# Optimization experiments

Measured on AMD Instinct MI355X. Metric: run time of the kernel, lower is better.

## Reference

```python
import jax, jax.numpy as jnp
import numpy as np

B, N, M = 8, 512, 6          # batch, num_roads, max_action
ED, SRC, OBS = 8, 64, 32     # edge_dim, source_obs_dim, obs_dim
D, H = 16, 64                # out_dim (fixed in source), MLPBase hidden


def setup_inputs() -> dict:
    key = jax.random.key(0)
    ks = jax.random.split(key, 24)
    p = lambda k, sh, s=0.05: (jax.random.normal(k, sh) * s).astype(jnp.float32)
    inp = {}
    inp['obs'] = jax.random.normal(ks[0], (B, SRC), dtype=jnp.float32)
    inp['obs_all'] = jax.random.normal(ks[1], (B, N, OBS), dtype=jnp.float32)
    inp['edge_attrs'] = jax.random.normal(ks[2], (B, N, N, ED), dtype=jnp.float32)
    inp['ridxs'] = jax.random.randint(ks[3], (B,), 0, N)
    idxs = jax.random.randint(ks[4], (N, M), 0, N)
    masks = jax.random.randint(ks[5], (N, M), 0, 2)
    inp['road_neighbor_idxs'] = idxs
    inp['road_neighbor_masks'] = masks
    # A[i, j] = 1 iff i is a (masked-valid) neighbor of j
    cols = jnp.repeat(jnp.arange(N), M)
    inp['A'] = jnp.zeros((N, N), jnp.float32).at[idxs.reshape(-1), cols].max(
        masks.reshape(-1).astype(jnp.float32))
    inp['PA'] = jnp.full((N, N), 1e-6, jnp.float32)
    # parameters (stored as (in, out); y = x @ W + b)
    inp['w_src'] = p(ks[6], (SRC, D * M)); inp['b_src'] = jnp.zeros((D * M,), jnp.float32)
    inp['w_obs'] = p(ks[7], (OBS, D));     inp['b_obs'] = jnp.zeros((D,), jnp.float32)
    inp['res_w'] = p(ks[8], (2, D, D));    inp['res_b'] = jnp.zeros((2, D), jnp.float32)
    inp['ge_we'] = p(ks[9], (2, ED, D));   inp['ge_be'] = jnp.zeros((2, D), jnp.float32)
    inp['ge_wemb'] = p(ks[10], (2, 3 * D, D)); inp['ge_bemb'] = jnp.zeros((2, D), jnp.float32)
    inp['gated_w'] = p(ks[11], (2 * D * M, 2 * D)); inp['gated_b'] = jnp.zeros((2 * D,), jnp.float32)
    inp['base_w1'] = p(ks[12], (D, H));    inp['base_b1'] = jnp.zeros((H,), jnp.float32)
    inp['base_w2'] = p(ks[13], (H, H));    inp['base_b2'] = jnp.zeros((H,), jnp.float32)
    inp['act_w'] = p(ks[14], (H, M));      inp['act_b'] = jnp.zeros((M,), jnp.float32)
    return inp


def _edge_conv_gat(x, edge_attrs, adj, we, be, wemb, bemb):
    """EdgeConvGat: emb(cat[x_i, x_j, edge_map(e)]) aggregated by adj.
    emb is linear, so split its weight and avoid the (B,N,N,3D) concat:
      sum_j adj[bij] * (x_i W1 + x_j W2 + e_ij W3 + b)
    """
    W1, W2, W3 = wemb[:D], wemb[D:2 * D], wemb[2 * D:]
    e = edge_attrs @ we + be                      # (B,N,N,D)
    ep = e @ W3                                   # (B,N,N,D)
    deg = adj.sum(-1)                             # (B,N) row-sums of adj
    return ((x @ W1) * deg[..., None]
            + jnp.einsum('bij,bjk->bik', adj, x @ W2)
            + jnp.einsum('bij,bijk->bik', adj, ep)
            + bemb * deg[..., None])


def reference(obs, obs_all, edge_attrs, ridxs, road_neighbor_idxs,
              road_neighbor_masks, A, PA, w_src, b_src, w_obs, b_obs,
              res_w, res_b, ge_we, ge_be, ge_wemb, ge_bemb,
              gated_w, gated_b, base_w1, base_b1, base_w2, base_b2,
              act_w, act_b):
    # source_obs_map / obs_map (mean_field=1 -> full obs_all)
    obs_p = obs @ w_src + b_src                   # (B, D*M)
    x = obs_all @ w_obs + b_obs                   # (B, N, D)
    # adaptive adjacency (training=False -> dropout is identity)
    adj = jnp.broadcast_to(A + PA, (obs.shape[0], N, N))
    # graph conv loop (source overwrites obs_all_adaptive each iter from the
    # same x, faithfully reproduced; only the last iteration feeds the output)
    x_adapt = x
    for i in range(2):
        res = x @ res_w[i] + res_b[i]
        agg = _edge_conv_gat(x, edge_attrs, adj, ge_we[i], ge_be[i],
                             ge_wemb[i], ge_bemb[i])
        x_adapt = jax.nn.relu(res + agg)
    # gather per-road neighbor features and mask invalid slots to -1
    idx = road_neighbor_idxs[ridxs]               # (B, M)
    mask = road_neighbor_masks[ridxs]             # (B, M)
    sel = jnp.take_along_axis(x_adapt, idx[:, :, None], axis=1)  # (B, M, D)
    sel = jnp.where(mask[..., None] == 0, -1.0, sel).reshape(obs.shape[0], -1)
    # gated fusion + MLPBase (2-layer MLP stand-in) + action head
    g = jnp.concatenate([obs_p, sel], axis=-1) @ gated_w + gated_b
    gated, gate = jnp.split(g, 2, axis=-1)
    h = gated * jax.nn.sigmoid(gate)
    h = jax.nn.relu(h @ base_w1 + base_b1)
    h = jax.nn.relu(h @ base_w2 + base_b2)        # F.relu(self.base(...))
    return h @ act_w + act_b                      # (B, M) action values
```

## Files before the change

kernel.cpp:

```cpp
#include <hip/hip_runtime.h>
#include <math.h>


constexpr int Bc   = 8;
constexpr int Nc   = 512;
constexpr int Mc   = 6;
constexpr int EDc  = 8;
constexpr int SRCc = 64;
constexpr int OBSc = 32;
constexpr int Dc   = 16;
constexpr int Hc   = 64;

__global__ __launch_bounds__(512) void anmodel_kernel(
    const float* __restrict__ obs,
    const float* __restrict__ obs_all,
    const float* __restrict__ edge_attrs,
    const int*   __restrict__ ridxs,
    const int*   __restrict__ rni,
    const int*   __restrict__ rnm,
    const float* __restrict__ A,
    const float* __restrict__ PA,
    const float* __restrict__ w_src,
    const float* __restrict__ b_src,
    const float* __restrict__ w_obs,
    const float* __restrict__ b_obs,
    const float* __restrict__ res_w,
    const float* __restrict__ res_b,
    const float* __restrict__ ge_we,
    const float* __restrict__ ge_be,
    const float* __restrict__ ge_wemb,
    const float* __restrict__ ge_bemb,
    const float* __restrict__ gated_w,
    const float* __restrict__ gated_b,
    const float* __restrict__ base_w1,
    const float* __restrict__ base_b1,
    const float* __restrict__ base_w2,
    const float* __restrict__ base_b2,
    const float* __restrict__ act_w,
    const float* __restrict__ act_b,
    float* __restrict__ out)
{
    const int b    = blockIdx.x;
    const int tid  = threadIdx.x;
    const int lane = tid & 63;
    const int wave = tid >> 6;

    __shared__ float s_y[Nc][Dc];
    __shared__ float s_wobs[OBSc][Dc];
    __shared__ float s_bobs[Dc];
    __shared__ float s_W1[Dc][Dc];
    __shared__ float s_W2[Dc][Dc];
    __shared__ float s_resw[Dc][Dc];
    __shared__ float s_resb[Dc];
    __shared__ float s_we3[EDc][Dc];
    __shared__ float s_be3[Dc];
    __shared__ float s_bemb[Dc];
    __shared__ float s_sel[Mc * Dc];
    __shared__ float s_obsp[SRCc + 32];
    __shared__ float s_h0[Dc];
    __shared__ float s_h1[Hc];
    __shared__ float s_h2[Hc];

    const float* wemb1 = ge_wemb + 3 * Dc * Dc;
    for (int t = tid; t < OBSc * Dc; t += 512) s_wobs[t / Dc][t % Dc] = w_obs[t];
    for (int t = tid; t < Dc; t += 512) {
        s_bobs[t] = b_obs[t];
        s_resb[t] = res_b[Dc + t];
        s_bemb[t] = ge_bemb[Dc + t];
        float acc = 0.f;
        #pragma unroll
        for (int k = 0; k < Dc; ++k)
            acc = fmaf(ge_be[Dc + k], wemb1[(2 * Dc + k) * Dc + t], acc);
        s_be3[t] = acc;
    }
    for (int t = tid; t < Dc * Dc; t += 512) {
        s_W1[t / Dc][t % Dc]   = wemb1[t];
        s_W2[t / Dc][t % Dc]   = wemb1[Dc * Dc + t];
        s_resw[t / Dc][t % Dc] = res_w[Dc * Dc + t];
    }
    for (int t = tid; t < EDc * Dc; t += 512) {
        const int e = t / Dc, d = t % Dc;
        float acc = 0.f;
        #pragma unroll
        for (int k = 0; k < Dc; ++k)
            acc = fmaf(ge_we[EDc * Dc + e * Dc + k], wemb1[(2 * Dc + k) * Dc + d], acc);
        s_we3[e][d] = acc;
    }
    __syncthreads();

    {
        const int j = tid;
        const float* oa = obs_all + ((size_t)b * Nc + j) * OBSc;
        float o[OBSc];
        #pragma unroll
        for (int k = 0; k < OBSc; k += 4) {
            const float4 v = *reinterpret_cast<const float4*>(oa + k);
            o[k] = v.x; o[k + 1] = v.y; o[k + 2] = v.z; o[k + 3] = v.w;
        }
        float xv[Dc];
        #pragma unroll
        for (int d = 0; d < Dc; ++d) xv[d] = s_bobs[d];
        #pragma unroll
        for (int k = 0; k < OBSc; ++k) {
            const float ok = o[k];
            #pragma unroll
            for (int d = 0; d < Dc; ++d) xv[d] = fmaf(ok, s_wobs[k][d], xv[d]);
        }
        #pragma unroll
        for (int d = 0; d < Dc; ++d) {
            float acc = 0.f;
            #pragma unroll
            for (int k = 0; k < Dc; ++k) acc = fmaf(xv[k], s_W2[k][d], acc);
            s_y[j][d] = acc;
        }
    }
    __syncthreads();

    if (wave < Mc) {
        const int m  = wave;
        const int r  = ridxs[b];
        const int i  = rni[r * Mc + m];
        const int mk = rnm[r * Mc + m];
        const float* Arow = A  + (size_t)i * Nc;
        const float* Prow = PA + (size_t)i * Nc;

        float dv = 0.f;
        #pragma unroll
        for (int t = 0; t < 8; ++t) {
            const int j = lane * 8 + t;
            dv += Arow[j] + Prow[j];
        }
        #pragma unroll
        for (int s = 1; s < 64; s <<= 1) dv += __shfl_xor(dv, s);

        const int dq = lane & 15, jg = lane >> 4;
        float adot = 0.f;
        for (int t = 0; t < Nc / 4; ++t) {
            const int j = t * 4 + jg;
            adot = fmaf(Arow[j] + Prow[j], s_y[j][dq], adot);
        }
        adot += __shfl_xor(adot, 16);
        adot += __shfl_xor(adot, 32);

        const int e8 = lane & 7, jg8 = lane >> 3;
        const float* Erow = edge_attrs + (((size_t)b * Nc + i) * Nc) * EDc;
        float ag = 0.f;
        for (int t = 0; t < Nc / 8; ++t) {
            const int j = t * 8 + jg8;
            ag = fmaf(Arow[j] + Prow[j], Erow[(size_t)j * EDc + e8], ag);
        }
        ag += __shfl_xor(ag, 8);
        ag += __shfl_xor(ag, 16);
        ag += __shfl_xor(ag, 32);
        float agv[EDc];
        #pragma unroll
        for (int e = 0; e < EDc; ++e) agv[e] = __shfl(ag, e);

        const float* oa = obs_all + ((size_t)b * Nc + i) * OBSc;
        float xi[Dc];
        #pragma unroll
        for (int d = 0; d < Dc; ++d) xi[d] = s_bobs[d];
        for (int k = 0; k < OBSc; ++k) {
            const float ok = oa[k];
            #pragma unroll
            for (int d = 0; d < Dc; ++d) xi[d] = fmaf(ok, s_wobs[k][d], xi[d]);
        }

        if (lane < Dc) {
            const int d = lane;
            float resv = s_resb[d];
            float w1t  = 0.f;
            #pragma unroll
            for (int k = 0; k < Dc; ++k) {
                resv = fmaf(xi[k], s_resw[k][d], resv);
                w1t  = fmaf(xi[k], s_W1[k][d], w1t);
            }
            float agdot = 0.f;
            #pragma unroll
            for (int e = 0; e < EDc; ++e) agdot = fmaf(agv[e], s_we3[e][d], agdot);
            float aggv = fmaf(w1t, dv, adot) + agdot + dv * s_be3[d] + s_bemb[d] * dv;
            float xa = resv + aggv;
            xa = xa > 0.f ? xa : 0.f;
            s_sel[m * Dc + d] = (mk == 0) ? -1.0f : xa;
        }
    } else if (wave == 6) {
        for (int t = lane; t < SRCc + 32; t += 64) {
            float acc = b_src[t];
            for (int s = 0; s < SRCc; ++s)
                acc = fmaf(obs[b * SRCc + s], w_src[s * 96 + t], acc);
            s_obsp[t] = acc;
        }
    }
    __syncthreads();

    if (wave == 0) {
        float gv = 0.f;
        if (lane < 32) {
            gv = gated_b[lane];
            for (int t = 0; t < 96; ++t) gv = fmaf(s_obsp[t], gated_w[t * 32 + lane], gv);
            for (int t = 0; t < 96; ++t) gv = fmaf(s_sel[t],  gated_w[(96 + t) * 32 + lane], gv);
        }
        const float gate = __shfl(gv, (lane & 15) + 16);
        if (lane < Dc) {
            s_h0[lane] = gv * (1.0f / (1.0f + expf(-gate)));
        }
    }
    __syncthreads();
    if (wave == 0) {
        float acc = base_b1[lane];
        #pragma unroll
        for (int k = 0; k < Dc; ++k) acc = fmaf(s_h0[k], base_w1[k * Hc + lane], acc);
        s_h1[lane] = acc > 0.f ? acc : 0.f;
    }
    __syncthreads();
    if (wave == 0) {
        float acc = base_b2[lane];
        #pragma unroll
        for (int k = 0; k < Hc; ++k) acc = fmaf(s_h1[k], base_w2[k * Hc + lane], acc);
        s_h2[lane] = acc > 0.f ? acc : 0.f;
    }
    __syncthreads();
    if (wave == 0 && lane < Mc) {
        float acc = act_b[lane];
        #pragma unroll
        for (int k = 0; k < Hc; ++k) acc = fmaf(s_h2[k], act_w[k * Mc + lane], acc);
        out[b * Mc + lane] = acc;
    }
}

extern "C" void kernel_launch(void* const* d_in, const int* in_sizes, int n_in,
                              void* d_out, int out_size, void* d_ws, size_t ws_size,
                              hipStream_t stream) {
    (void)in_sizes; (void)n_in; (void)d_ws; (void)ws_size; (void)out_size;
    anmodel_kernel<<<dim3(Bc), dim3(512), 0, stream>>>(
        (const float*)d_in[0],  (const float*)d_in[1],  (const float*)d_in[2],
        (const int*)  d_in[3],  (const int*)  d_in[4],  (const int*)  d_in[5],
        (const float*)d_in[6],  (const float*)d_in[7],  (const float*)d_in[8],
        (const float*)d_in[9],  (const float*)d_in[10], (const float*)d_in[11],
        (const float*)d_in[12], (const float*)d_in[13], (const float*)d_in[14],
        (const float*)d_in[15], (const float*)d_in[16], (const float*)d_in[17],
        (const float*)d_in[18], (const float*)d_in[19], (const float*)d_in[20],
        (const float*)d_in[21], (const float*)d_in[22], (const float*)d_in[23],
        (const float*)d_in[24], (const float*)d_in[25],
        (float*)d_out);
}
```

Measured before the change: 160.1 us.

## Stage adjacency rows in LDS and defer W2 projection after aggregation

All threads now load the six needed A+PA rows into shared memory with coalesced reads, replacing the repeated per-wave global reads of A and PA. Node features x are stored directly, and the W2 projection is applied once to the aggregated vector instead of per node, so each thread skips a 16x16 matvec. The x_i recompute reuses s_x instead of reloading obs_all. The obs projection is spread over two waves, and several loops get unroll pragmas. This adds a 12KB shared buffer and a few extra shuffles.

```diff
diff --git a/kernel.cpp b/kernel.cpp
--- a/kernel.cpp
+++ b/kernel.cpp
@@ -45,7 +45,8 @@
     const int lane = tid & 63;
     const int wave = tid >> 6;
 
-    __shared__ float s_y[Nc][Dc];
+    __shared__ float s_x[Nc][Dc];
+    __shared__ float s_w[Mc][Nc];
     __shared__ float s_wobs[OBSc][Dc];
     __shared__ float s_bobs[Dc];
     __shared__ float s_W1[Dc][Dc];
@@ -55,6 +56,8 @@
     __shared__ float s_we3[EDc][Dc];
     __shared__ float s_be3[Dc];
     __shared__ float s_bemb[Dc];
+    __shared__ int   s_idx[Mc];
+    __shared__ int   s_msk[Mc];
     __shared__ float s_sel[Mc * Dc];
     __shared__ float s_obsp[SRCc + 32];
     __shared__ float s_h0[Dc];
@@ -86,6 +89,11 @@
             acc = fmaf(ge_we[EDc * Dc + e * Dc + k], wemb1[(2 * Dc + k) * Dc + d], acc);
         s_we3[e][d] = acc;
     }
+    if (tid < Mc) {
+        const int r = ridxs[b];
+        s_idx[tid] = rni[r * Mc + tid];
+        s_msk[tid] = rnm[r * Mc + tid];
+    }
     __syncthreads();
 
     {
@@ -107,47 +115,46 @@
             for (int d = 0; d < Dc; ++d) xv[d] = fmaf(ok, s_wobs[k][d], xv[d]);
         }
         #pragma unroll
-        for (int d = 0; d < Dc; ++d) {
-            float acc = 0.f;
-            #pragma unroll
-            for (int k = 0; k < Dc; ++k) acc = fmaf(xv[k], s_W2[k][d], acc);
-            s_y[j][d] = acc;
-        }
+        for (int d = 0; d < Dc; ++d) s_x[j][d] = xv[d];
+    }
+    #pragma unroll
+    for (int m = 0; m < Mc; ++m) {
+        const int i = s_idx[m];
+        s_w[m][tid] = A[(size_t)i * Nc + tid] + PA[(size_t)i * Nc + tid];
     }
     __syncthreads();
 
     if (wave < Mc) {
-        const int m  = wave;
-        const int r  = ridxs[b];
-        const int i  = rni[r * Mc + m];
-        const int mk = rnm[r * Mc + m];
-        const float* Arow = A  + (size_t)i * Nc;
-        const float* Prow = PA + (size_t)i * Nc;
+        const int m = wave;
+        const float* __restrict__ wrow = &s_w[m][0];
 
         float dv = 0.f;
         #pragma unroll
-        for (int t = 0; t < 8; ++t) {
-            const int j = lane * 8 + t;
-            dv += Arow[j] + Prow[j];
-        }
+        for (int t = 0; t < Nc / 64; ++t) dv += wrow[t * 64 + lane];
         #pragma unroll
         for (int s = 1; s < 64; s <<= 1) dv += __shfl_xor(dv, s);
 
         const int dq = lane & 15, jg = lane >> 4;
-        float adot = 0.f;
+        float wx = 0.f;
+        #pragma unroll 8
         for (int t = 0; t < Nc / 4; ++t) {
             const int j = t * 4 + jg;
-            adot = fmaf(Arow[j] + Prow[j], s_y[j][dq], adot);
-        }
-        adot += __shfl_xor(adot, 16);
-        adot += __shfl_xor(adot, 32);
+            wx = fmaf(wrow[j], s_x[j][dq], wx);
+        }
+        wx += __shfl_xor(wx, 16);
+        wx += __shfl_xor(wx, 32);
+        float wxv[Dc];
+        #pragma unroll
+        for (int k = 0; k < Dc; ++k) wxv[k] = __shfl(wx, k);
 
         const int e8 = lane & 7, jg8 = lane >> 3;
-        const float* Erow = edge_attrs + (((size_t)b * Nc + i) * Nc) * EDc;
+        const int i  = s_idx[m];
+        const float* __restrict__ Erow = edge_attrs + (((size_t)b * Nc + i) * Nc) * EDc;
         float ag = 0.f;
+        #pragma unroll 4
         for (int t = 0; t < Nc / 8; ++t) {
             const int j = t * 8 + jg8;
-            ag = fmaf(Arow[j] + Prow[j], Erow[(size_t)j * EDc + e8], ag);
+            ag = fmaf(wrow[j], Erow[(size_t)j * EDc + e8], ag);
         }
         ag += __shfl_xor(ag, 8);
         ag += __shfl_xor(ag, 16);
@@ -156,36 +163,31 @@
         #pragma unroll
         for (int e = 0; e < EDc; ++e) agv[e] = __shfl(ag, e);
 
-        const float* oa = obs_all + ((size_t)b * Nc + i) * OBSc;
-        float xi[Dc];
-        #pragma unroll
-        for (int d = 0; d < Dc; ++d) xi[d] = s_bobs[d];
-        for (int k = 0; k < OBSc; ++k) {
-            const float ok = oa[k];
-            #pragma unroll
-            for (int d = 0; d < Dc; ++d) xi[d] = fmaf(ok, s_wobs[k][d], xi[d]);
-        }
-
         if (lane < Dc) {
             const int d = lane;
             float resv = s_resb[d];
             float w1t  = 0.f;
+            float adot = 0.f;
             #pragma unroll
             for (int k = 0; k < Dc; ++k) {
-                resv = fmaf(xi[k], s_resw[k][d], resv);
-                w1t  = fmaf(xi[k], s_W1[k][d], w1t);
+                const float xik = s_x[i][k];
+                resv = fmaf(xik, s_resw[k][d], resv);
+                w1t  = fmaf(xik, s_W1[k][d], w1t);
+                adot = fmaf(wxv[k], s_W2[k][d], adot);
             }
             float agdot = 0.f;
             #pragma unroll
             for (int e = 0; e < EDc; ++e) agdot = fmaf(agv[e], s_we3[e][d], agdot);
-            float aggv = fmaf(w1t, dv, adot) + agdot + dv * s_be3[d] + s_bemb[d] * dv;
+            float aggv = fmaf(w1t, dv, adot) + agdot + dv * (s_be3[d] + s_bemb[d]);
             float xa = resv + aggv;
             xa = xa > 0.f ? xa : 0.f;
-            s_sel[m * Dc + d] = (mk == 0) ? -1.0f : xa;
-        }
-    } else if (wave == 6) {
-        for (int t = lane; t < SRCc + 32; t += 64) {
+            s_sel[m * Dc + d] = (s_msk[m] == 0) ? -1.0f : xa;
+        }
+    } else {
+        const int t = (wave - 6) * 64 + lane;
+        if (t < SRCc + 32) {
             float acc = b_src[t];
+            #pragma unroll 8
             for (int s = 0; s < SRCc; ++s)
                 acc = fmaf(obs[b * SRCc + s], w_src[s * 96 + t], acc);
             s_obsp[t] = acc;
```

Result: faster. 151.9 us (-5.1%).
